# Kernel tuning notes

Hardware: AMD Instinct MI355X
Metric: run time of the kernel (lower is better)

## Reference

```python
import jax, jax.numpy as jnp
import numpy as np

EPS = 1e-5
GROUPS = 8


def setup_inputs() -> dict:
    key = jax.random.key(0)
    ks = jax.random.split(key, 7)
    B, C, H, W = 4, 512, 64, 64
    x = jax.random.normal(ks[0], (B, C, H, W), dtype=jnp.float32)
    gn_w = jax.random.normal(ks[1], (C,), dtype=jnp.float32) * 0.02 + 1.0
    gn_b = jax.random.normal(ks[2], (C,), dtype=jnp.float32) * 0.02
    # 1x1 convs stored as [out, in] matrices
    qkv_w = jax.random.normal(ks[3], (3 * C, C), dtype=jnp.float32) * (C ** -0.5)
    qkv_b = jax.random.normal(ks[4], (3 * C,), dtype=jnp.float32) * 0.02
    proj_w = jax.random.normal(ks[5], (C, C), dtype=jnp.float32) * (C ** -0.5)
    proj_b = jax.random.normal(ks[6], (C,), dtype=jnp.float32) * 0.02
    return {"x": x, "gn_w": gn_w, "gn_b": gn_b, "qkv_w": qkv_w,
            "qkv_b": qkv_b, "proj_w": proj_w, "proj_b": proj_b}


def _group_norm(x, w, b):
    B, C, H, W = x.shape
    xg = x.reshape(B, GROUPS, C // GROUPS, H, W)
    mu = jnp.mean(xg, axis=(2, 3, 4), keepdims=True)
    var = jnp.var(xg, axis=(2, 3, 4), keepdims=True)
    xn = ((xg - mu) * jax.lax.rsqrt(var + EPS)).reshape(B, C, H, W)
    return xn * w[None, :, None, None] + b[None, :, None, None]


def reference(x, gn_w, gn_b, qkv_w, qkv_b, proj_w, proj_b):
    B, C, H, W = x.shape
    N = H * W
    scale = C ** (-0.5)
    h = _group_norm(x, gn_w, gn_b)
    # 1x1 conv -> [B, 3C, N]
    qkv = jnp.einsum('oc,bcn->bon', qkv_w, h.reshape(B, C, N)) + qkv_b[None, :, None]
    q, k, v = jnp.split(qkv, 3, axis=1)  # each [B, C, N]
    # scores[b, n, m] = sum_c q[b,c,n] * k[b,c,m]
    attn = jax.nn.softmax(jnp.einsum('bcn,bcm->bnm', q, k) * scale, axis=-1)
    # out[b,c,n] = sum_m v[b,c,m] * attn[b,n,m]   (v @ attn^T)
    hout = jnp.einsum('bcm,bnm->bcn', v, attn)
    proj = jnp.einsum('oc,bcn->bon', proj_w, hout) + proj_b[None, :, None]
    return x + proj.reshape(B, C, H, W)
```

## Files before the change

kernel.cpp:

```cpp
#include <hip/hip_runtime.h>
#include <math.h>

#define SCALE 0.044194173824159216f
#define QI 28.22222222f
#define K8SCL ((4.5f/127.0f)*(4.5f/127.0f)*SCALE)
#define K8SCL2 (K8SCL * 1.4426950408889634f)
#define PSCL 0.49609375f
#define VSCL 0.035433070866141736f

typedef __bf16 bf16x8 __attribute__((ext_vector_type(8)));
typedef float  f32x4  __attribute__((ext_vector_type(4)));
typedef int    i32x4  __attribute__((ext_vector_type(4)));
typedef unsigned int u32;

__device__ __forceinline__ void gload16(const void* g, void* l) {
    __builtin_amdgcn_global_load_lds(
        (const __attribute__((address_space(1))) u32*)g,
        (__attribute__((address_space(3))) u32*)l, 16, 0, 0);
}

__global__ __launch_bounds__(256) void gn_part_w(const float* __restrict__ x,
                                                 float* __restrict__ part,
                                                 const float* __restrict__ qw,
                                                 const float* __restrict__ pwsrc,
                                                 __bf16* __restrict__ wdst) {
    if (blockIdx.x >= 512) {
        int i = ((blockIdx.x - 512)*256 + threadIdx.x) * 4;
        #pragma unroll
        for (int rep = 0; rep < 4; ++rep, i += 262144) {
            const float* src = (i < 786432) ? (qw + i) : (pwsrc + (i - 786432));
            float4 v = *(const float4*)src;
            wdst[i+0] = (__bf16)v.x; wdst[i+1] = (__bf16)v.y;
            wdst[i+2] = (__bf16)v.z; wdst[i+3] = (__bf16)v.w;
        }
        return;
    }
    int gi = blockIdx.x >> 4, sl = blockIdx.x & 15;
    const float4* p = (const float4*)(x + (size_t)gi * 64 * 4096) + (size_t)sl * 4096;
    float s = 0.f, ss = 0.f;
    #pragma unroll 4
    for (int i = threadIdx.x; i < 4096; i += 256) {
        float4 v = p[i];
        s  += v.x + v.y + v.z + v.w;
        ss += v.x*v.x + v.y*v.y + v.z*v.z + v.w*v.w;
    }
    __shared__ float rs[256], rss[256];
    rs[threadIdx.x] = s; rss[threadIdx.x] = ss;
    __syncthreads();
    for (int o = 128; o > 0; o >>= 1) {
        if (threadIdx.x < o) { rs[threadIdx.x] += rs[threadIdx.x+o]; rss[threadIdx.x] += rss[threadIdx.x+o]; }
        __syncthreads();
    }
    if (threadIdx.x == 0) {
        part[blockIdx.x*2 + 0] = rs[0];
        part[blockIdx.x*2 + 1] = rss[0];
    }
}

__global__ __launch_bounds__(64) void gn_fin(const float* __restrict__ part,
                                             float* __restrict__ stats) {
    int t = threadIdx.x;
    if (t < 32) {
        float s = 0.f, ss = 0.f;
        #pragma unroll
        for (int i = 0; i < 16; ++i) { s += part[(t*16+i)*2]; ss += part[(t*16+i)*2+1]; }
        float inv = 1.0f / (float)(64 * 4096);
        float mu  = s * inv;
        float var = ss * inv - mu * mu;
        stats[t*2 + 0] = mu;
        stats[t*2 + 1] = rsqrtf(var + 1e-5f);
    }
}

__global__ __launch_bounds__(256) void gn_apply_t(const float* __restrict__ x,
                                                  const float* __restrict__ stats,
                                                  const float* __restrict__ gw,
                                                  const float* __restrict__ gb,
                                                  __bf16* __restrict__ hT) {
    __shared__ __bf16 tile[64][88];
    int b = blockIdx.z, c0 = blockIdx.y * 64, n0 = blockIdx.x * 64;
    int t = threadIdx.x;
    float mu  = stats[(b*8 + blockIdx.y)*2];
    float rsg = stats[(b*8 + blockIdx.y)*2 + 1];
    int c = t >> 2, ns = t & 3;
    float a = gw[c0+c] * rsg;
    float d = gb[c0+c] - mu * a;
    const float* xr = x + ((size_t)b*512 + c0 + c)*4096 + n0 + ns*16;
    #pragma unroll
    for (int e4 = 0; e4 < 4; ++e4) {
        float4 v = *(const float4*)(xr + e4*4);
        tile[ns*16 + e4*4 + 0][c] = (__bf16)(v.x*a + d);
        tile[ns*16 + e4*4 + 1][c] = (__bf16)(v.y*a + d);
        tile[ns*16 + e4*4 + 2][c] = (__bf16)(v.z*a + d);
        tile[ns*16 + e4*4 + 3][c] = (__bf16)(v.w*a + d);
    }
    __syncthreads();
    int n = t >> 2, cs = t & 3;
    __bf16* dst = hT + ((size_t)b*4096 + n0 + n)*512 + c0 + cs*16;
    *(uint4*)(dst)     = *(const uint4*)(&tile[n][cs*16]);
    *(uint4*)(dst + 8) = *(const uint4*)(&tile[n][cs*16 + 8]);
}

template<int MODE>
__global__ __launch_bounds__(256) void mm128(
        const __bf16* __restrict__ A, int lda, size_t sA,
        const __bf16* __restrict__ B, int ldb, size_t sB,
        int Kdim,
        const float* __restrict__ bias,
        const float* __restrict__ res, size_t sR,
        void* __restrict__ out, int ldo, size_t sO) {
    __shared__ __bf16 As[3][128][32];
    __shared__ __bf16 Bs[3][128][32];

    const int t = threadIdx.x, w = t >> 6, l = t & 63;
    const int l15 = l & 15, lq = l >> 4;
    const int bz = blockIdx.z;

    const int gx = gridDim.x;
    int lin = blockIdx.y * gx + blockIdx.x;
    {
        const int nwg = gx * gridDim.y;
        const int qn = nwg >> 3, rn = nwg & 7;
        const int xcd = lin & 7, idx = lin >> 3;
        const int base = (xcd < rn) ? xcd*(qn+1) : rn*(qn+1) + (xcd-rn)*qn;
        lin = base + idx;
    }
    const int j0 = (lin % gx) * 128;
    const int i0 = (lin / gx) * 128;

    const __bf16* Ab = A + sA*bz;
    const __bf16* Bb = B + sB*bz;
    const int rowblk = (w & 1)*64;
    const int colblk = (w >> 1)*64;

    const int slot0 = w*64 + l;
    const int rowS0 = slot0 >> 2;
    const int rowS1 = rowS0 + 64;
    const int csS   = (((slot0 & 3) ^ ((rowS0 >> 1) & 3))) * 8;
    const int off0  = (w*64)*16;
    const int off1  = (256 + w*64)*16;

    f32x4 acc[4][4];
    #pragma unroll
    for (int mr = 0; mr < 4; ++mr)
        #pragma unroll
        for (int nr = 0; nr < 4; ++nr)
            #pragma unroll
            for (int r = 0; r < 4; ++r) acc[mr][nr][r] = 0.f;

    auto STAGE = [&](int kc, int bi) {
        char* Ad = (char*)As[bi];
        char* Bd = (char*)Bs[bi];
        gload16(Ab + (size_t)(i0 + rowS0)*lda + kc + csS, Ad + off0);
        gload16(Ab + (size_t)(i0 + rowS1)*lda + kc + csS, Ad + off1);
        gload16(Bb + (size_t)(j0 + rowS0)*ldb + kc + csS, Bd + off0);
        gload16(Bb + (size_t)(j0 + rowS1)*ldb + kc + csS, Bd + off1);
    };

    const int rsw = (l15 >> 1) & 3;
    const int koff = (lq ^ rsw) << 4;

    const int nch = Kdim >> 5;
    STAGE(0, 0);
    STAGE(32, 1);

    for (int cc = 0; cc < nch; ++cc) {
        if (cc < nch - 1) asm volatile("s_waitcnt vmcnt(4)\n\ts_barrier" ::: "memory");
        else              asm volatile("s_waitcnt vmcnt(0)\n\ts_barrier" ::: "memory");

        const char* Ac = (const char*)As[cc % 3];
        const char* Bc = (const char*)Bs[cc % 3];
        bf16x8 av[4], bv[4];
        #pragma unroll
        for (int mr = 0; mr < 4; ++mr)
            av[mr] = *(const bf16x8*)(Ac + (rowblk + mr*16 + l15)*64 + koff);
        #pragma unroll
        for (int nr = 0; nr < 4; ++nr)
            bv[nr] = *(const bf16x8*)(Bc + (colblk + nr*16 + l15)*64 + koff);
        if (cc + 2 < nch) STAGE((cc + 2)*32, (cc + 2) % 3);
        #pragma unroll
        for (int mr = 0; mr < 4; ++mr)
            #pragma unroll
            for (int nr = 0; nr < 4; ++nr)
                acc[mr][nr] = __builtin_amdgcn_mfma_f32_16x16x32_bf16(av[mr], bv[nr], acc[mr][nr], 0, 0, 0);
    }

    #pragma unroll
    for (int mr = 0; mr < 4; ++mr)
        #pragma unroll
        for (int nr = 0; nr < 4; ++nr) {
            int col = j0 + colblk + nr*16 + l15;
            #pragma unroll
            for (int r = 0; r < 4; ++r) {
                int lrow = rowblk + mr*16 + lq*4 + r;
                int gi = i0 + lrow;
                float v = acc[mr][nr][r];
                if constexpr (MODE == 1) {
                    v += bias[gi];
                    int q = __float2int_rn(v * QI);
                    q = q < -127 ? -127 : (q > 127 ? 127 : q);
                    ((char*)out)[sO*bz + (size_t)gi*ldo + col] = (char)q;
                } else {
                    v += bias[gi] + res[sR*bz + (size_t)gi*ldo + col];
                    ((float*)out)[sO*bz + (size_t)gi*ldo + col] = v;
                }
            }
        }
}

template<int M> struct AccT { using T = f32x4; };
template<> struct AccT<4> { using T = i32x4; };
template<> struct AccT<5> { using T = i32x4; };

#define LDSB (98304 + 4096)
template<int MODE>
__global__ __launch_bounds__(512) void mm256(
        const void* __restrict__ A, int ldaB, size_t sAB,
        const void* __restrict__ B, int ldbB, size_t sBB,
        int Kbytes,
        const float* __restrict__ bias,
        void* __restrict__ out, int ldo, size_t sO,
        float* __restrict__ rowpart) {
    extern __shared__ char smem[];
    char*  Abase = smem;
    char*  Bbase = smem + 49152;
    float* redp  = (float*)(smem + 98304);

    const int t = threadIdx.x, w = t >> 6, l = t & 63;
    const int l15 = l & 15, lq = l >> 4;
    const int bz = (MODE == 4) ? (blockIdx.z >> 2) : blockIdx.z;
    const int kh = (MODE == 4) ? (blockIdx.z & 3) : 0;
    const size_t kbase = (size_t)kh * Kbytes;

    const int gx = gridDim.x;
    int lin = blockIdx.y * gx + blockIdx.x;
    {
        const int nwg = gx * gridDim.y;
        const int qn = nwg >> 3, rn = nwg & 7;
        const int xcd = lin & 7, idx = lin >> 3;
        const int base = (xcd < rn) ? xcd*(qn+1) : rn*(qn+1) + (xcd-rn)*qn;
        lin = base + idx;
    }
    const int j0 = (lin % gx) * 256;
    const int i0 = (lin / gx) * 256;

    const char* Ab = (const char*)A + sAB*bz + kbase;
    const char* Bb = (const char*)B + sBB*bz + kbase;
    const int wr = w & 1;
    const int wc = w >> 1;

    const int slot0 = w*64 + l;
    const int rowS0 = slot0 >> 2;
    const int rowS1 = rowS0 + 128;
    const int csS   = (((slot0 & 3) ^ ((rowS0 >> 1) & 3))) * 16;
    const int off0  = (w*64)*16;
    const int off1  = (512 + w*64)*16;

    typename AccT<MODE>::T acc[8][4];
    #pragma unroll
    for (int mr = 0; mr < 8; ++mr)
        #pragma unroll
        for (int nr = 0; nr < 4; ++nr)
            #pragma unroll
            for (int r = 0; r < 4; ++r) acc[mr][nr][r] = 0;

    auto STAGE = [&](int kc, int bi) {
        char* Ad = Abase + bi*16384;
        char* Bd = Bbase + bi*16384;
        gload16(Ab + (size_t)(i0 + rowS0)*ldaB + kc + csS, Ad + off0);
        gload16(Ab + (size_t)(i0 + rowS1)*ldaB + kc + csS, Ad + off1);
        gload16(Bb + (size_t)(j0 + rowS0)*ldbB + kc + csS, Bd + off0);
        gload16(Bb + (size_t)(j0 + rowS1)*ldbB + kc + csS, Bd + off1);
    };

    const int rsw = (l15 >> 1) & 3;
    const int koff = (lq ^ rsw) << 4;

    const int nch = Kbytes >> 6;
    STAGE(0, 0);
    STAGE(64, 1);

    for (int cc = 0; cc < nch; ++cc) {
        if (cc < nch - 1) asm volatile("s_waitcnt vmcnt(4)\n\ts_barrier" ::: "memory");
        else              asm volatile("s_waitcnt vmcnt(0)\n\ts_barrier" ::: "memory");

        const char* Ac = Abase + (cc % 3)*16384;
        const char* Bc = Bbase + (cc % 3)*16384;
        i32x4 araw[8], braw[4];
        #pragma unroll
        for (int mr = 0; mr < 8; ++mr)
            araw[mr] = *(const i32x4*)(Ac + (wr*128 + mr*16 + l15)*64 + koff);
        #pragma unroll
        for (int nr = 0; nr < 4; ++nr)
            braw[nr] = *(const i32x4*)(Bc + (wc*64 + nr*16 + l15)*64 + koff);
        if (cc + 2 < nch) STAGE((cc + 2)*64, (cc + 2) % 3);
        #pragma unroll
        for (int mr = 0; mr < 8; ++mr)
            #pragma unroll
            for (int nr = 0; nr < 4; ++nr) {
                if constexpr (MODE == 4 || MODE == 5) {
                    acc[mr][nr] = __builtin_amdgcn_mfma_i32_16x16x64_i8(
                        araw[mr], braw[nr], acc[mr][nr], 0, 0, 0);
                } else {
                    acc[mr][nr] = __builtin_amdgcn_mfma_f32_16x16x32_bf16(
                        __builtin_bit_cast(bf16x8, araw[mr]),
                        __builtin_bit_cast(bf16x8, braw[nr]), acc[mr][nr], 0, 0, 0);
                }
            }
    }

    if constexpr (MODE == 5) {
        const int jblk = j0 >> 8;
        float rpart[8][4];
        #pragma unroll
        for (int mr = 0; mr < 8; ++mr)
            #pragma unroll
            for (int r = 0; r < 4; ++r) rpart[mr][r] = 0.f;
        #pragma unroll
        for (int mr = 0; mr < 8; ++mr)
            #pragma unroll
            for (int nr = 0; nr < 4; ++nr) {
                int col = j0 + wc*64 + nr*16 + l15;
                #pragma unroll
                for (int r = 0; r < 4; ++r) {
                    int row = wr*128 + mr*16 + lq*4 + r;
                    float e = exp2f((float)acc[mr][nr][r] * K8SCL2);
                    int q = __float2int_rn(e * PSCL);
                    if (q > 127) q = 127;
                    ((char*)out)[sO*bz + (size_t)(i0 + row)*ldo + col] = (char)q;
                    rpart[mr][r] += (float)q;
                }
            }
        #pragma unroll
        for (int m = 1; m < 16; m <<= 1)
            #pragma unroll
            for (int mr = 0; mr < 8; ++mr)
                #pragma unroll
                for (int r = 0; r < 4; ++r)
                    rpart[mr][r] += __shfl_xor(rpart[mr][r], m);
        __syncthreads();
        if (l15 == 0) {
            #pragma unroll
            for (int mr = 0; mr < 8; ++mr)
                #pragma unroll
                for (int r = 0; r < 4; ++r)
                    redp[(wr*128 + mr*16 + lq*4 + r)*4 + wc] = rpart[mr][r];
        }
        __syncthreads();
        if (t < 256)
            rowpart[(size_t)bz*131072 + (size_t)jblk*4096 + i0 + t] =
                redp[t*4+0] + redp[t*4+1] + redp[t*4+2] + redp[t*4+3];
        return;
    }

    #pragma unroll
    for (int mr = 0; mr < 8; ++mr)
        #pragma unroll
        for (int nr = 0; nr < 4; ++nr) {
            int col = j0 + wc*64 + nr*16 + l15;
            #pragma unroll
            for (int r = 0; r < 4; ++r) {
                int lrow = wr*128 + mr*16 + lq*4 + r;
                if constexpr (MODE == 0) {
                    float v = (float)acc[mr][nr][r] + bias[col];
                    int q = __float2int_rn(v * QI);
                    q = q < -127 ? -127 : (q > 127 ? 127 : q);
                    char* qk = (char*)out + (size_t)bz*8388608;
                    size_t row = (size_t)(i0 + lrow);
                    char* p = (col < 512) ? (qk + row*512 + col)
                                          : (qk + 2097152 + row*512 + (col - 512));
                    *p = (char)q;
                } else {
                    __bf16* po = (__bf16*)out + sO*bz + (size_t)kh*2097152;
                    po[(size_t)(i0 + lrow)*ldo + col] = (__bf16)(float)acc[mr][nr][r];
                }
            }
        }
}

__global__ __launch_bounds__(256) void pv_reduce(const __bf16* __restrict__ part,
                                                 const float* __restrict__ rowpart,
                                                 __bf16* __restrict__ OT) {
    int b = blockIdx.y, r0 = blockIdx.x * 16;
    __shared__ float rs[16];
    int t = threadIdx.x;
    if (t < 16) {
        const float* rp = rowpart + (size_t)b*131072 + r0 + t;
        float s = 0.f;
        #pragma unroll
        for (int jb = 0; jb < 16; ++jb) s += rp[jb*4096];
        rs[t] = VSCL / s;
    }
    __syncthreads();
    int row = r0 + (t >> 4), cseg = (t & 15) * 32;
    const __bf16* p0 = part + (size_t)b*16777216 + (size_t)row*512 + cseg;
    __bf16* o = OT + (size_t)b*2097152 + (size_t)row*512 + cseg;
    float sc = rs[t >> 4];
    #pragma unroll
    for (int g = 0; g < 4; ++g) {
        bf16x8 a0 = *(const bf16x8*)(p0 + g*8);
        bf16x8 a1 = *(const bf16x8*)(p0 + 2097152 + g*8);
        bf16x8 a2 = *(const bf16x8*)(p0 + 4194304 + g*8);
        bf16x8 a3 = *(const bf16x8*)(p0 + 6291456 + g*8);
        bf16x8 r;
        #pragma unroll
        for (int e = 0; e < 8; ++e)
            r[e] = (__bf16)((((float)a0[e] + (float)a1[e]) + ((float)a2[e] + (float)a3[e])) * sc);
        *(bf16x8*)(o + g*8) = r;
    }
}

extern "C" void kernel_launch(void* const* d_in, const int* in_sizes, int n_in,
                              void* d_out, int out_size, void* d_ws, size_t ws_size,
                              hipStream_t stream) {
    const float* x      = (const float*)d_in[0];
    const float* gn_w   = (const float*)d_in[1];
    const float* gn_b   = (const float*)d_in[2];
    const float* qkv_w  = (const float*)d_in[3];
    const float* qkv_b  = (const float*)d_in[4];
    const float* proj_w = (const float*)d_in[5];
    const float* proj_b = (const float*)d_in[6];

    char* w8 = (char*)d_ws;
    char*   v8buf = w8 + 33554432;
    __bf16* OT   = (__bf16*)(w8 + 50331648);
    __bf16* wq   = (__bf16*)(w8 + 67108864);
    __bf16* pw   = (__bf16*)(w8 + 68681728);
    float*  rowpart = (float*)(w8 + 69206016);
    float*  part = (float*)(w8 + 71303168);
    float*  st   = (float*)(w8 + 71307264);
    const size_t baseP = 71307520ULL;
    __bf16* hT   = (__bf16*)(w8 + baseP);

    size_t avail = (ws_size > baseP) ? (ws_size - baseP) : 0;
    int cap = (int)(avail / 33554432ULL);
    if (cap < 1) cap = 1;
    if (cap > 4) cap = 4;

    hipFuncSetAttribute((const void*)mm256<0>,
                        hipFuncAttributeMaxDynamicSharedMemorySize, LDSB);
    hipFuncSetAttribute((const void*)mm256<4>,
                        hipFuncAttributeMaxDynamicSharedMemorySize, LDSB);
    hipFuncSetAttribute((const void*)mm256<5>,
                        hipFuncAttributeMaxDynamicSharedMemorySize, LDSB);

    gn_part_w<<<768, 256, 0, stream>>>(x, part, qkv_w, proj_w, wq);
    gn_fin<<<1, 64, 0, stream>>>(part, st);
    gn_apply_t<<<dim3(64, 8, 4), 256, 0, stream>>>(x, st, gn_w, gn_b, hT);

    mm256<0><<<dim3(4, 16, 4), 512, LDSB, stream>>>(
        hT, 1024, (size_t)4096*1024, wq, 1024, 0, 1024,
        qkv_b, w8, 0, 0, nullptr);
    mm128<1><<<dim3(32, 4, 4), 256, 0, stream>>>(
        wq + (size_t)1024*512, 512, 0, hT, 512, (size_t)4096*512, 512,
        qkv_b + 1024, nullptr, 0, v8buf, 4096, (size_t)512*4096);

    for (int b0 = 0; b0 < 4; b0 += cap) {
        int c = (4 - b0 < cap) ? (4 - b0) : cap;
        char* Pb = w8 + baseP + (size_t)b0*33554432;
        mm256<5><<<dim3(16, 16, c), 512, LDSB, stream>>>(
            w8 + (size_t)b0*8388608, 512, 8388608,
            w8 + (size_t)b0*8388608 + 2097152, 512, 8388608, 512,
            nullptr, Pb, 4096, 33554432,
            rowpart + (size_t)b0*131072);
        mm256<4><<<dim3(2, 16, c*4), 512, LDSB, stream>>>(
            Pb, 4096, 33554432,
            v8buf + (size_t)b0*2097152, 4096, 2097152, 1024,
            nullptr, Pb + 16777216, 512, 16777216,
            nullptr);
        pv_reduce<<<dim3(256, c), 256, 0, stream>>>(
            (const __bf16*)(Pb + 16777216), rowpart + (size_t)b0*131072,
            OT + (size_t)b0*2097152);
    }

    mm128<2><<<dim3(32, 4, 4), 256, 0, stream>>>(
        pw, 512, 0, OT, 512, (size_t)4096*512, 512,
        proj_b, x, (size_t)512*4096, (float*)d_out, 4096, (size_t)512*4096);
}
```

Baseline: 209.1 us.

## Swap GEMM operand roles so epilogue stores pack four bytes per lane

```diff
diff --git a/kernel.cpp b/kernel.cpp
--- a/kernel.cpp
+++ b/kernel.cpp
@@ -4,11 +4,11 @@
 #define SCALE 0.044194173824159216f
 #define QI 28.22222222f
 #define K8SCL ((4.5f/127.0f)*(4.5f/127.0f)*SCALE)
-#define K8SCL2 (K8SCL * 1.4426950408889634f)
 #define PSCL 0.49609375f
 #define VSCL 0.035433070866141736f
 
 typedef __bf16 bf16x8 __attribute__((ext_vector_type(8)));
+typedef __bf16 bf16x4 __attribute__((ext_vector_type(4)));
 typedef float  f32x4  __attribute__((ext_vector_type(4)));
 typedef int    i32x4  __attribute__((ext_vector_type(4)));
 typedef unsigned int u32;
@@ -310,72 +310,83 @@
     }
 
     if constexpr (MODE == 5) {
-        const int jblk = j0 >> 8;
-        float rpart[8][4];
-        #pragma unroll
-        for (int mr = 0; mr < 8; ++mr)
-            #pragma unroll
-            for (int r = 0; r < 4; ++r) rpart[mr][r] = 0.f;
-        #pragma unroll
-        for (int mr = 0; mr < 8; ++mr)
+        const int kblk = i0 >> 8;
+        float rpart[4] = {0.f, 0.f, 0.f, 0.f};
+        #pragma unroll
+        for (int mr = 0; mr < 8; ++mr) {
+            int key0 = i0 + wr*128 + mr*16 + lq*4;
             #pragma unroll
             for (int nr = 0; nr < 4; ++nr) {
-                int col = j0 + wc*64 + nr*16 + l15;
+                int q = j0 + wc*64 + nr*16 + l15;
+                u32 pk = 0;
                 #pragma unroll
                 for (int r = 0; r < 4; ++r) {
-                    int row = wr*128 + mr*16 + lq*4 + r;
-                    float e = exp2f((float)acc[mr][nr][r] * K8SCL2);
-                    int q = __float2int_rn(e * PSCL);
-                    if (q > 127) q = 127;
-                    ((char*)out)[sO*bz + (size_t)(i0 + row)*ldo + col] = (char)q;
-                    rpart[mr][r] += (float)q;
+                    float e = __expf((float)acc[mr][nr][r] * K8SCL);
+                    int qv = __float2int_rn(e * PSCL);
+                    if (qv > 127) qv = 127;
+                    pk |= ((u32)qv) << (8*r);
+                    rpart[nr] += (float)qv;
                 }
+                *(u32*)((char*)out + sO*bz + (size_t)q*4096 + key0) = pk;
             }
-        #pragma unroll
-        for (int m = 1; m < 16; m <<= 1)
-            #pragma unroll
-            for (int mr = 0; mr < 8; ++mr)
-                #pragma unroll
-                for (int r = 0; r < 4; ++r)
-                    rpart[mr][r] += __shfl_xor(rpart[mr][r], m);
-        __syncthreads();
-        if (l15 == 0) {
-            #pragma unroll
-            for (int mr = 0; mr < 8; ++mr)
-                #pragma unroll
-                for (int r = 0; r < 4; ++r)
-                    redp[(wr*128 + mr*16 + lq*4 + r)*4 + wc] = rpart[mr][r];
+        }
+        #pragma unroll
+        for (int nr = 0; nr < 4; ++nr) {
+            rpart[nr] += __shfl_xor(rpart[nr], 16);
+            rpart[nr] += __shfl_xor(rpart[nr], 32);
+        }
+        if (lq == 0) {
+            #pragma unroll
+            for (int nr = 0; nr < 4; ++nr)
+                redp[(wc*64 + nr*16 + l15)*2 + wr] = rpart[nr];
         }
         __syncthreads();
         if (t < 256)
-            rowpart[(size_t)bz*131072 + (size_t)jblk*4096 + i0 + t] =
-                redp[t*4+0] + redp[t*4+1] + redp[t*4+2] + redp[t*4+3];
+            rowpart[(size_t)bz*131072 + (size_t)kblk*4096 + j0 + t] =
+                redp[t*2] + redp[t*2+1];
         return;
     }
 
-    #pragma unroll
-    for (int mr = 0; mr < 8; ++mr)
-        #pragma unroll
-        for (int nr = 0; nr < 4; ++nr) {
-            int col = j0 + wc*64 + nr*16 + l15;
-            #pragma unroll
-            for (int r = 0; r < 4; ++r) {
-                int lrow = wr*128 + mr*16 + lq*4 + r;
-                if constexpr (MODE == 0) {
-                    float v = (float)acc[mr][nr][r] + bias[col];
-                    int q = __float2int_rn(v * QI);
-                    q = q < -127 ? -127 : (q > 127 ? 127 : q);
-                    char* qk = (char*)out + (size_t)bz*8388608;
-                    size_t row = (size_t)(i0 + lrow);
-                    char* p = (col < 512) ? (qk + row*512 + col)
-                                          : (qk + 2097152 + row*512 + (col - 512));
-                    *p = (char)q;
-                } else {
-                    __bf16* po = (__bf16*)out + sO*bz + (size_t)kh*2097152;
-                    po[(size_t)(i0 + lrow)*ldo + col] = (__bf16)(float)acc[mr][nr][r];
+    if constexpr (MODE == 0) {
+        char* qk = (char*)out + (size_t)bz*8388608;
+        #pragma unroll
+        for (int mr = 0; mr < 8; ++mr) {
+            int o0 = i0 + wr*128 + mr*16 + lq*4;
+            float4 b4 = *(const float4*)(bias + o0);
+            float bb[4] = {b4.x, b4.y, b4.z, b4.w};
+            char* half = (o0 < 512) ? qk : (qk + 2097152 - 512);
+            #pragma unroll
+            for (int nr = 0; nr < 4; ++nr) {
+                int n = j0 + wc*64 + nr*16 + l15;
+                u32 pk = 0;
+                #pragma unroll
+                for (int r = 0; r < 4; ++r) {
+                    float v = (float)acc[mr][nr][r] + bb[r];
+                    int qv = __float2int_rn(v * QI);
+                    qv = qv < -127 ? -127 : (qv > 127 ? 127 : qv);
+                    pk |= ((u32)(unsigned char)(char)qv) << (8*r);
                 }
+                *(u32*)(half + (size_t)n*512 + o0) = pk;
             }
         }
+        return;
+    }
+
+    {
+        __bf16* po = (__bf16*)out + sO*bz + (size_t)kh*2097152;
+        #pragma unroll
+        for (int mr = 0; mr < 8; ++mr) {
+            int c0 = i0 + wr*128 + mr*16 + lq*4;
+            #pragma unroll
+            for (int nr = 0; nr < 4; ++nr) {
+                int q = j0 + wc*64 + nr*16 + l15;
+                bf16x4 pv;
+                #pragma unroll
+                for (int r = 0; r < 4; ++r) pv[r] = (__bf16)(float)acc[mr][nr][r];
+                *(bf16x4*)(po + (size_t)q*512 + c0) = pv;
+            }
+        }
+    }
 }
 
 __global__ __launch_bounds__(256) void pv_reduce(const __bf16* __restrict__ part,
@@ -448,8 +459,8 @@
     gn_fin<<<1, 64, 0, stream>>>(part, st);
     gn_apply_t<<<dim3(64, 8, 4), 256, 0, stream>>>(x, st, gn_w, gn_b, hT);
 
-    mm256<0><<<dim3(4, 16, 4), 512, LDSB, stream>>>(
-        hT, 1024, (size_t)4096*1024, wq, 1024, 0, 1024,
+    mm256<0><<<dim3(16, 4, 4), 512, LDSB, stream>>>(
+        wq, 1024, 0, hT, 1024, (size_t)4096*1024, 1024,
         qkv_b, w8, 0, 0, nullptr);
     mm128<1><<<dim3(32, 4, 4), 256, 0, stream>>>(
         wq + (size_t)1024*512, 512, 0, hT, 512, (size_t)4096*512, 512,
@@ -459,13 +470,13 @@
         int c = (4 - b0 < cap) ? (4 - b0) : cap;
         char* Pb = w8 + baseP + (size_t)b0*33554432;
         mm256<5><<<dim3(16, 16, c), 512, LDSB, stream>>>(
-            w8 + (size_t)b0*8388608, 512, 8388608,
-            w8 + (size_t)b0*8388608 + 2097152, 512, 8388608, 512,
+            w8 + (size_t)b0*8388608 + 2097152, 512, 8388608,
+            w8 + (size_t)b0*8388608, 512, 8388608, 512,
             nullptr, Pb, 4096, 33554432,
             rowpart + (size_t)b0*131072);
-        mm256<4><<<dim3(2, 16, c*4), 512, LDSB, stream>>>(
-            Pb, 4096, 33554432,
-            v8buf + (size_t)b0*2097152, 4096, 2097152, 1024,
+        mm256<4><<<dim3(16, 2, c*4), 512, LDSB, stream>>>(
+            v8buf + (size_t)b0*2097152, 4096, 2097152,
+            Pb, 4096, 33554432, 1024,
             nullptr, Pb + 16777216, 512, 16777216,
             nullptr);
         pv_reduce<<<dim3(256, c), 256, 0, stream>>>(
```

Measured after the change: 214.3 us. 1.02x slower.
